# Performance work log

Hardware: AMD Instinct MI355X
Metric: run time of the kernel (lower is better)

## Reference

```python
import jax, jax.numpy as jnp
import numpy as np

EPS = 1e-6
SIGMA = 1.0       # get_matrix default sigma
INIT_SIGMA = 1.0  # args.init_sigma


def setup_inputs() -> dict:
    key = jax.random.key(0)
    ks = jax.random.split(key, 12)
    B, T, LD, NB = 16, 2048, 256, 32
    s = 1.0 / np.sqrt(LD)
    E_raw = jax.random.normal(ks[5], (LD, LD), jnp.float32)
    E_w, _ = jnp.linalg.qr(E_raw)  # orthogonal like geotorch.orthogonal
    return {
        "Z": jax.random.normal(ks[0], (B, T, LD), jnp.float32),
        "obs_times": jax.random.uniform(ks[1], (B, T, 1), jnp.float32),
        "D": jax.random.normal(ks[2], (NB, LD), jnp.float32),
        "coeff_W": jax.random.normal(ks[3], (NB, LD), jnp.float32) * s,
        "coeff_b": jnp.zeros((NB,), jnp.float32),
        "E_w": E_w.astype(jnp.float32),
        "B_w": jax.random.normal(ks[6], (LD, LD), jnp.float32) * s,
        "C_w": jax.random.normal(ks[7], (LD, LD), jnp.float32) * s,
        "M_w": jax.random.normal(ks[8], (LD, LD), jnp.float32) * s,
        "init_mean_p": jax.random.normal(ks[9], (LD,), jnp.float32),
        "init_log_var": jax.random.normal(ks[10], (LD,), jnp.float32),
        "y_log_var": jax.random.normal(ks[11], (LD,), jnp.float32),
    }


def _binop(qi, qj):
    # (A_j*A_i, Bu_j + A_j*Bu_i): combine earlier element qi with later qj
    A_i, Bu_i = qi
    A_j, Bu_j = qj
    return (A_j * A_i, Bu_j + A_j * Bu_i)


def reference(Z, obs_times, D, coeff_W, coeff_b, E_w, B_w, C_w, M_w,
              init_mean_p, init_log_var, y_log_var):
    LD = Z.shape[-1]
    # alphas = B(Z)
    alphas = jnp.einsum('btd,ed->bte', Z, B_w)                      # (B,T,LD)
    # get_matrix (vectorized over batch and time)
    A_basis = -(jnp.exp(D) + EPS)                                   # (NB,LD), negative
    A_coeff = jax.nn.softmax(jnp.einsum('btd,nd->btn', alphas, coeff_W) + coeff_b, axis=-1)
    A_mat = jnp.einsum('btn,nd->btd', A_coeff, A_basis)             # (B,T,LD)
    exp_A_m = jnp.exp(A_mat * obs_times)                            # mean transition
    exp_B_m = (exp_A_m - 1.0) / A_mat * alphas
    exp_A_v = jnp.exp(2.0 * A_mat * obs_times)                      # var transition
    exp_B_v = 0.5 * SIGMA ** 2 * (exp_A_v - 1.0) / A_mat + EPS
    mats_A = jnp.concatenate([exp_A_m, exp_A_v], axis=-1)           # (B,T,2LD)
    mats_B = jnp.concatenate([exp_B_m, exp_B_v], axis=-1)           # (B,T,2LD)
    # parallel linear-recurrence scan over time
    cum_A, cum_B = jax.lax.associative_scan(_binop, (mats_A, mats_B), axis=1)
    # initial condition in rotated coordinates
    init_mean0 = E_w.T @ init_mean_p                                # (LD,)
    diag_v = INIT_SIGMA * (jnp.exp(init_log_var) + EPS)
    init_var0 = jnp.einsum('ki,k->i', E_w ** 2, diag_v)             # diag(E^T diag(v) E)
    init_mv = jnp.concatenate([init_mean0, init_var0], axis=0)      # (2LD,)
    imv = cum_A * init_mv                                           # (B,T,2LD)
    init_mean, init_var = imv[..., :LD], imv[..., LD:]
    xs_mean, xs_var = cum_B[..., :LD], cum_B[..., LD:]
    y_var = jnp.exp(y_log_var) + EPS
    # output projections: M(E(.)) and history C(E(Z))
    history = jnp.einsum('btd,ed,fe->btf', Z, E_w, C_w)
    means = jnp.einsum('btd,ed,fe->btf', xs_mean + init_mean, E_w, M_w) + history
    stds = jnp.einsum('btd,ed,fe->btf', jnp.sqrt(xs_var + init_var + y_var), E_w, M_w)
    return means, stds, alphas
```

## Files before the change

kernel.cpp:

```cpp
#include <hip/hip_runtime.h>
#include <math.h>

#define EPS 1e-6f

#define B_   16
#define T_   2048
#define LD   256
#define NB   32
#define BT   (B_ * T_)
#define NCH  64
#define CHUNK (T_ / NCH)

typedef short bf16x8 __attribute__((ext_vector_type(8)));
typedef float f32x4  __attribute__((ext_vector_type(4)));

__device__ __forceinline__ unsigned short f2b(float f) {
    unsigned int u = __float_as_uint(f);
    unsigned int r = (u + 0x7fffu + ((u >> 16) & 1u)) >> 16;
    return (unsigned short)r;
}

__device__ __forceinline__ float b2f(unsigned short h) {
    return __uint_as_float(((unsigned int)h) << 16);
}

__device__ __forceinline__ void gl_lds16(const void* g, void* l) {
    __builtin_amdgcn_global_load_lds(
        (const __attribute__((address_space(1))) unsigned int*)g,
        (__attribute__((address_space(3))) unsigned int*)l, 16, 0, 0);
}

__device__ __forceinline__ int xcd_map(int wg) {
    int x = wg & 7, s = wg >> 3;
    return (s & 3) | (x << 2) | ((s >> 2) << 5);
}

__device__ __forceinline__ void stage_tile(const unsigned short* __restrict__ src,
                                           int row0, int stride, int kb,
                                           unsigned short* lds, int wv, int lane) {
#pragma unroll
    for (int cc = 0; cc < 2; ++cc) {
        int c = wv * 2 + cc;
        int r = c * 16 + (lane >> 2);
        int qd = (lane & 3) ^ ((r >> 1) & 3);
        const unsigned short* g = src + (size_t)(row0 + r) * stride + kb + qd * 8;
        gl_lds16(g, lds + c * 512);
    }
}

__device__ __forceinline__ bf16x8 frag_ld(const unsigned short* lds, int row, int qd) {
    int pq = qd ^ ((row >> 1) & 3);
    return *(const bf16x8*)(lds + row * 32 + pq * 8);
}

__device__ __forceinline__ int u_idx(int i, int d) {
    return ((d >> 5) << 10) + (i << 5) + (((((d >> 3) & 3)) ^ (i & 3)) << 3) + (d & 7);
}

__global__ __launch_bounds__(256) void k_pre(const float* __restrict__ Z,
                                             const float* __restrict__ Dm,
                                             const float* __restrict__ cw,
                                             const float* __restrict__ Ew,
                                             const float* __restrict__ Bw,
                                             const float* __restrict__ Cw,
                                             const float* __restrict__ Mw,
                                             const float* __restrict__ imp,
                                             const float* __restrict__ ilv,
                                             const float* __restrict__ ylv,
                                             unsigned short* __restrict__ GMh,
                                             unsigned short* __restrict__ GCh,
                                             unsigned short* __restrict__ cwbh,
                                             float* __restrict__ im0,
                                             float* __restrict__ iv0,
                                             float* __restrict__ yv,
                                             unsigned short* __restrict__ AbTh,
                                             unsigned short* __restrict__ AbTl,
                                             unsigned short* __restrict__ Bwh,
                                             unsigned short* __restrict__ Zh) {
    int bid = blockIdx.x;
    int tid = threadIdx.x;
    if (bid < 544) {
        const float* W; const float* E; unsigned short* out; int d0, f0;
        if (bid < 256)      { W = Mw; E = Ew; out = GMh;  d0 = (bid & 15) * 16; f0 = (bid >> 4) * 16; }
        else if (bid < 512) { W = Cw; E = Ew; out = GCh;  d0 = (bid & 15) * 16; f0 = ((bid - 256) >> 4) * 16; }
        else                { W = cw; E = Bw; out = cwbh; d0 = (bid & 15) * 16; f0 = ((bid - 512) >> 4) * 16; }
        __shared__ float Ws[16][17];
        __shared__ float Es[16][17];
        int tx = tid & 15, ty = tid >> 4;
        float acc = 0.f;
        for (int eb = 0; eb < LD; eb += 16) {
            Ws[ty][tx] = W[(f0 + ty) * LD + eb + tx];
            Es[ty][tx] = E[(eb + ty) * LD + d0 + tx];
            __syncthreads();
#pragma unroll
            for (int k = 0; k < 16; ++k) acc = fmaf(Ws[ty][k], Es[k][tx], acc);
            __syncthreads();
        }
        out[(f0 + ty) * LD + d0 + tx] = f2b(acc);
    } else if (bid < 577) {
        int sub = bid - 544;
        int t = tid;
        if (sub == 0) {
            float sm = 0.f, sv = 0.f;
            for (int k = 0; k < LD; ++k) {
                float e = Ew[k * LD + t];
                sm = fmaf(e, imp[k], sm);
                sv = fmaf(e * e, expf(ilv[k]) + EPS, sv);
            }
            im0[t] = sm;
            iv0[t] = sv;
            yv[t]  = expf(ylv[t]) + EPS;
        } else {
            int n = sub - 1;
            float a = -(expf(Dm[n * LD + t]) + EPS);
            unsigned short h = f2b(a);
            AbTh[t * NB + n] = h;
            AbTl[t * NB + n] = f2b(a - b2f(h));
        }
    } else if (bid < 641) {
        int i = (bid - 577) * 256 + tid;
        float4 v = ((const float4*)Bw)[i];
        ((ushort4*)Bwh)[i] = make_ushort4(f2b(v.x), f2b(v.y), f2b(v.z), f2b(v.w));
    } else {
        int i = (bid - 641) * 256 + tid;
        float4 v = ((const float4*)Z)[i];
        ((ushort4*)Zh)[i] = make_ushort4(f2b(v.x), f2b(v.y), f2b(v.z), f2b(v.w));
    }
}

__global__ __launch_bounds__(256) void k_zb(const unsigned short* __restrict__ Zh,
                                            const unsigned short* __restrict__ Bwh,
                                            const unsigned short* __restrict__ cwbh,
                                            const float* __restrict__ cb,
                                            float* __restrict__ alphas,
                                            float* __restrict__ logits) {
    __shared__ unsigned short As[128 * 32];
    __shared__ unsigned short Bs[128 * 32];
    int tid = threadIdx.x, lane = tid & 63, wv = tid >> 6;
    int m0 = blockIdx.x * 128;
    int y  = blockIdx.y;
    if (y < 2) {
        int n0 = y * 128;
        int wm = (wv & 1) * 64, wn = (wv >> 1) * 64;
        f32x4 acc[4][4];
#pragma unroll
        for (int i = 0; i < 4; ++i)
#pragma unroll
            for (int j = 0; j < 4; ++j) acc[i][j] = (f32x4){0.f, 0.f, 0.f, 0.f};
        for (int kb = 0; kb < LD; kb += 32) {
            stage_tile(Zh, m0, LD, kb, As, wv, lane);
            stage_tile(Bwh, n0, LD, kb, Bs, wv, lane);
            __syncthreads();
            int qd = lane >> 4;
            bf16x8 af[4], bf[4];
#pragma unroll
            for (int i = 0; i < 4; ++i) af[i] = frag_ld(As, wm + i * 16 + (lane & 15), qd);
#pragma unroll
            for (int j = 0; j < 4; ++j) bf[j] = frag_ld(Bs, wn + j * 16 + (lane & 15), qd);
#pragma unroll
            for (int i = 0; i < 4; ++i)
#pragma unroll
                for (int j = 0; j < 4; ++j)
                    acc[i][j] = __builtin_amdgcn_mfma_f32_16x16x32_bf16(af[i], bf[j], acc[i][j], 0, 0, 0);
            __syncthreads();
        }
        int col = wn + (lane & 15);
        int rb  = wm + ((lane >> 4) << 2);
#pragma unroll
        for (int i = 0; i < 4; ++i)
#pragma unroll
            for (int j = 0; j < 4; ++j)
#pragma unroll
                for (int r = 0; r < 4; ++r)
                    alphas[(size_t)(m0 + rb + i * 16 + r) * LD + n0 + col + j * 16] = acc[i][j][r];
    } else {
        f32x4 acc[2][2];
#pragma unroll
        for (int i = 0; i < 2; ++i)
#pragma unroll
            for (int j = 0; j < 2; ++j) acc[i][j] = (f32x4){0.f, 0.f, 0.f, 0.f};
        for (int kb = 0; kb < LD; kb += 32) {
            stage_tile(Zh, m0, LD, kb, As, wv, lane);
            if (wv < 2) {
                int r = wv * 16 + (lane >> 2);
                int qd = (lane & 3) ^ ((r >> 1) & 3);
                gl_lds16(cwbh + (size_t)r * LD + kb + qd * 8, Bs + wv * 512);
            }
            __syncthreads();
            int qd = lane >> 4;
            bf16x8 af[2], bff[2];
#pragma unroll
            for (int i = 0; i < 2; ++i) af[i] = frag_ld(As, wv * 32 + i * 16 + (lane & 15), qd);
#pragma unroll
            for (int j = 0; j < 2; ++j) bff[j] = frag_ld(Bs, j * 16 + (lane & 15), qd);
#pragma unroll
            for (int i = 0; i < 2; ++i)
#pragma unroll
                for (int j = 0; j < 2; ++j)
                    acc[i][j] = __builtin_amdgcn_mfma_f32_16x16x32_bf16(af[i], bff[j], acc[i][j], 0, 0, 0);
            __syncthreads();
        }
        int col = lane & 15;
        int rb  = (lane >> 4) << 2;
#pragma unroll
        for (int i = 0; i < 2; ++i)
#pragma unroll
            for (int j = 0; j < 2; ++j)
#pragma unroll
                for (int r = 0; r < 4; ++r) {
                    int row = m0 + wv * 32 + i * 16 + rb + r;
                    int cc  = j * 16 + col;
                    logits[(size_t)row * NB + cc] = acc[i][j][r] + cb[cc];
                }
    }
}

__global__ __launch_bounds__(256) void k_tot(const float* __restrict__ logits,
                                             const float* __restrict__ alphas,
                                             const float* __restrict__ obs,
                                             const unsigned short* __restrict__ AbTh,
                                             const unsigned short* __restrict__ AbTl,
                                             float* __restrict__ totA,
                                             float* __restrict__ totBm,
                                             float* __restrict__ totBv) {
    __shared__ unsigned int U[8192];
    __shared__ unsigned short Ph[1024];
    __shared__ unsigned short Pl[1024];
    int tid = threadIdx.x;
    int d = tid;
    int bid = xcd_map(blockIdx.x);
    int bt0 = bid * CHUNK;

    float av[32];
#pragma unroll
    for (int i = 0; i < 32; ++i) av[i] = alphas[(size_t)(bt0 + i) * LD + d];

    int l = tid & 31, rg = tid >> 5;
#pragma unroll
    for (int jj = 0; jj < 4; ++jj) {
        int row = rg * 4 + jj;
        float v = logits[(size_t)(bt0 + row) * NB + l];
        float mx = v;
#pragma unroll
        for (int off = 16; off >= 1; off >>= 1) mx = fmaxf(mx, __shfl_xor(mx, off, 32));
        float e = __expf(v - mx);
        float s = e;
#pragma unroll
        for (int off = 16; off >= 1; off >>= 1) s += __shfl_xor(s, off, 32);
        float p = e * __builtin_amdgcn_rcpf(s);
        unsigned short h = f2b(p);
        unsigned short lo = f2b(p - b2f(h));
        int sa = row * 32 + ((((l >> 3) ^ ((row >> 1) & 3))) << 3) + (l & 7);
        Ph[sa] = h;
        Pl[sa] = lo;
    }
    __syncthreads();

    int lane = tid & 63, wv = tid >> 6;
    int qd = lane >> 4, mr = lane & 15;
    bf16x8 ph[2], pl[2];
#pragma unroll
    for (int iT = 0; iT < 2; ++iT) {
        ph[iT] = frag_ld(Ph, iT * 16 + mr, qd);
        pl[iT] = frag_ld(Pl, iT * 16 + mr, qd);
    }
#pragma unroll
    for (int j = 0; j < 4; ++j) {
        int dcol = wv * 64 + j * 16 + mr;
        bf16x8 ah = *(const bf16x8*)(AbTh + dcol * NB + qd * 8);
        bf16x8 al = *(const bf16x8*)(AbTl + dcol * NB + qd * 8);
#pragma unroll
        for (int iT = 0; iT < 2; ++iT) {
            f32x4 acc = (f32x4){0.f, 0.f, 0.f, 0.f};
            acc = __builtin_amdgcn_mfma_f32_16x16x32_bf16(ph[iT], ah, acc, 0, 0, 0);
            acc = __builtin_amdgcn_mfma_f32_16x16x32_bf16(pl[iT], ah, acc, 0, 0, 0);
            acc = __builtin_amdgcn_mfma_f32_16x16x32_bf16(ph[iT], al, acc, 0, 0, 0);
#pragma unroll
            for (int r = 0; r < 4; ++r)
                U[u_idx(iT * 16 + qd * 4 + r, dcol)] = __float_as_uint(acc[r]);
        }
    }
    __syncthreads();

    float ra = 1.f, rm = 0.f, rv = 0.f;
    int ubase = ((d >> 5) << 10) + (d & 7);
    int qb = (d >> 3) & 3;
#pragma unroll
    for (int i = 0; i < CHUNK; ++i) {
        int ui = ubase + (i << 5) + ((qb ^ (i & 3)) << 3);
        float Am = __uint_as_float(U[ui]);
        float tt = obs[bt0 + i];
        float eAm = __expf(Am * tt);
        float ieA = __builtin_amdgcn_rcpf(Am);
        float e2  = eAm * eAm;
        float eBm = (eAm - 1.f) * ieA * av[i];
        float eBv = fmaf(0.5f * (e2 - 1.f), ieA, EPS);
        rm = fmaf(eAm, rm, eBm);
        rv = fmaf(e2, rv, eBv);
        ra *= eAm;
    }
    int pidx = bid * LD + d;
    totA[pidx] = ra; totBm[pidx] = rm; totBv[pidx] = rv;
}

__global__ __launch_bounds__(256) void k_chunkpfx(const float* __restrict__ totA,
                                                  const float* __restrict__ totBm,
                                                  const float* __restrict__ totBv,
                                                  float* __restrict__ preA,
                                                  float* __restrict__ preBm,
                                                  float* __restrict__ preBv) {
    int d = threadIdx.x;
    int b = blockIdx.x;
    float Pa = 1.f, Pm = 0.f, Pv = 0.f;
    for (int g = 0; g < 8; ++g) {
        float a8[8], m8[8], v8[8];
#pragma unroll
        for (int k = 0; k < 8; ++k) {
            int pidx = (b * NCH + g * 8 + k) * LD + d;
            a8[k] = totA[pidx]; m8[k] = totBm[pidx]; v8[k] = totBv[pidx];
        }
#pragma unroll
        for (int k = 0; k < 8; ++k) {
            int pidx = (b * NCH + g * 8 + k) * LD + d;
            preA[pidx] = Pa; preBm[pidx] = Pm; preBv[pidx] = Pv;
            Pm = fmaf(a8[k], Pm, m8[k]);
            Pv = fmaf(a8[k] * a8[k], Pv, v8[k]);
            Pa *= a8[k];
        }
    }
}

__global__ __launch_bounds__(256) void k_sms(const float* __restrict__ logits,
                                             const float* __restrict__ alphas,
                                             const float* __restrict__ obs,
                                             const unsigned short* __restrict__ AbTh,
                                             const unsigned short* __restrict__ AbTl,
                                             const float* __restrict__ preA,
                                             const float* __restrict__ preBm,
                                             const float* __restrict__ preBv,
                                             const float* __restrict__ im0,
                                             const float* __restrict__ iv0,
                                             const float* __restrict__ yv,
                                             const unsigned short* __restrict__ Zh,
                                             const unsigned short* __restrict__ GMh,
                                             const unsigned short* __restrict__ GCh,
                                             float* __restrict__ means,
                                             float* __restrict__ stds) {
    __shared__ unsigned int U[16384];
    unsigned short* Ph = (unsigned short*)U;
    unsigned short* Pl = (unsigned short*)(U + 1024);
    int tid = threadIdx.x, lane = tid & 63, wv = tid >> 6;
    int d = tid;
    int bt0 = blockIdx.x * 64;

    int l = tid & 31, rg = tid >> 5;
#pragma unroll
    for (int jj = 0; jj < 8; ++jj) {
        int row = rg * 8 + jj;
        float v = logits[(size_t)(bt0 + row) * NB + l];
        float mx = v;
#pragma unroll
        for (int off = 16; off >= 1; off >>= 1) mx = fmaxf(mx, __shfl_xor(mx, off, 32));
        float e = __expf(v - mx);
        float s = e;
#pragma unroll
        for (int off = 16; off >= 1; off >>= 1) s += __shfl_xor(s, off, 32);
        float p = e * __builtin_amdgcn_rcpf(s);
        unsigned short h = f2b(p);
        unsigned short lo = f2b(p - b2f(h));
        int sa = row * 32 + ((((l >> 3) ^ ((row >> 1) & 3))) << 3) + (l & 7);
        Ph[sa] = h;
        Pl[sa] = lo;
    }
    __syncthreads();

    int qd = lane >> 4, mr = lane & 15;
    bf16x8 ph[4], pl[4];
#pragma unroll
    for (int iT = 0; iT < 4; ++iT) {
        ph[iT] = frag_ld(Ph, iT * 16 + mr, qd);
        pl[iT] = frag_ld(Pl, iT * 16 + mr, qd);
    }
    __syncthreads();

#pragma unroll
    for (int j = 0; j < 4; ++j) {
        int dcol = wv * 64 + j * 16 + mr;
        bf16x8 ah = *(const bf16x8*)(AbTh + dcol * NB + qd * 8);
        bf16x8 al = *(const bf16x8*)(AbTl + dcol * NB + qd * 8);
#pragma unroll
        for (int iT = 0; iT < 4; ++iT) {
            f32x4 acc = (f32x4){0.f, 0.f, 0.f, 0.f};
            acc = __builtin_amdgcn_mfma_f32_16x16x32_bf16(ph[iT], ah, acc, 0, 0, 0);
            acc = __builtin_amdgcn_mfma_f32_16x16x32_bf16(pl[iT], ah, acc, 0, 0, 0);
            acc = __builtin_amdgcn_mfma_f32_16x16x32_bf16(ph[iT], al, acc, 0, 0, 0);
#pragma unroll
            for (int r = 0; r < 4; ++r) {
                int i = iT * 16 + qd * 4 + r;
                U[((i >> 5) << 13) + u_idx(i & 31, dcol)] = __float_as_uint(acc[r]);
            }
        }
    }
    __syncthreads();

    int p0 = (blockIdx.x * 2) * LD + d;
    float ga0 = preA[p0],      gm0 = preBm[p0],      gv0 = preBv[p0];
    float ga1 = preA[p0 + LD], gm1 = preBm[p0 + LD], gv1 = preBv[p0 + LD];
    float i0 = im0[d], v0 = iv0[d], yvd = yv[d];

    int ubase = ((d >> 5) << 10) + (d & 7);
    int qb = (d >> 3) & 3;
    for (int g = 0; g < 4; ++g) {
        float av0[8], av1[8];
#pragma unroll
        for (int k = 0; k < 8; ++k) {
            av0[k] = alphas[(size_t)(bt0 + g * 8 + k) * LD + d];
            av1[k] = alphas[(size_t)(bt0 + 32 + g * 8 + k) * LD + d];
        }
#pragma unroll
        for (int k = 0; k < 8; ++k) {
            int i = g * 8 + k;
            int ui0 = ubase + (i << 5) + ((qb ^ (i & 3)) << 3);
            int ui1 = 8192 + ui0;
            float Am0 = __uint_as_float(U[ui0]);
            float Am1 = __uint_as_float(U[ui1]);
            float t0 = obs[bt0 + i];
            float t1 = obs[bt0 + 32 + i];
            float e0 = __expf(Am0 * t0);
            float e1 = __expf(Am1 * t1);
            float r0 = __builtin_amdgcn_rcpf(Am0);
            float r1 = __builtin_amdgcn_rcpf(Am1);
            float q0 = e0 * e0, q1 = e1 * e1;
            float bm0 = (e0 - 1.f) * r0 * av0[k];
            float bm1 = (e1 - 1.f) * r1 * av1[k];
            float bv0 = fmaf(0.5f * (q0 - 1.f), r0, EPS);
            float bv1 = fmaf(0.5f * (q1 - 1.f), r1, EPS);
            gm0 = fmaf(e0, gm0, bm0);   gm1 = fmaf(e1, gm1, bm1);
            gv0 = fmaf(q0, gv0, bv0);   gv1 = fmaf(q1, gv1, bv1);
            ga0 *= e0;                  ga1 *= e1;
            float mm0 = fmaf(ga0, i0, gm0);
            float mm1 = fmaf(ga1, i0, gm1);
            float vv0 = fmaf(ga0 * ga0, v0, gv0) + yvd;
            float vv1 = fmaf(ga1 * ga1, v0, gv1) + yvd;
            float ss0 = sqrtf(vv0);
            float ss1 = sqrtf(vv1);
            U[ui0] = ((unsigned int)f2b(mm0) << 16) | (unsigned int)f2b(ss0);
            U[ui1] = ((unsigned int)f2b(mm1) << 16) | (unsigned int)f2b(ss1);
        }
    }
    __syncthreads();

    f32x4 accm[4][4], accs[4][4];
#pragma unroll
    for (int iT = 0; iT < 4; ++iT)
#pragma unroll
        for (int j = 0; j < 4; ++j) {
            accm[iT][j] = (f32x4){0.f, 0.f, 0.f, 0.f};
            accs[iT][j] = (f32x4){0.f, 0.f, 0.f, 0.f};
        }
    for (int kc = 0; kc < 8; ++kc) {
        bf16x8 am[4], asv[4], az[4];
#pragma unroll
        for (int iT = 0; iT < 4; ++iT) {
            int row = iT * 16 + mr;
            int ii = row & 31;
            int off = ((row >> 5) << 13) + (kc << 10) + (ii << 5) + ((qd ^ (ii & 3)) << 3);
            uint4 ua = *(const uint4*)(U + off);
            uint4 ub = *(const uint4*)(U + off + 4);
            unsigned int uu[8] = {ua.x, ua.y, ua.z, ua.w, ub.x, ub.y, ub.z, ub.w};
            bf16x8 m_, s_;
#pragma unroll
            for (int k = 0; k < 8; ++k) {
                m_[k] = (short)(uu[k] >> 16);
                s_[k] = (short)(uu[k] & 0xffffu);
            }
            am[iT] = m_; asv[iT] = s_;
            az[iT] = *(const bf16x8*)(Zh + (size_t)(bt0 + row) * LD + kc * 32 + qd * 8);
        }
#pragma unroll
        for (int j = 0; j < 4; ++j) {
            int brow = wv * 64 + j * 16 + mr;
            bf16x8 bm = *(const bf16x8*)(GMh + (size_t)brow * LD + kc * 32 + qd * 8);
            bf16x8 bc = *(const bf16x8*)(GCh + (size_t)brow * LD + kc * 32 + qd * 8);
#pragma unroll
            for (int iT = 0; iT < 4; ++iT) {
                accm[iT][j] = __builtin_amdgcn_mfma_f32_16x16x32_bf16(am[iT],  bm, accm[iT][j], 0, 0, 0);
                accs[iT][j] = __builtin_amdgcn_mfma_f32_16x16x32_bf16(asv[iT], bm, accs[iT][j], 0, 0, 0);
                accm[iT][j] = __builtin_amdgcn_mfma_f32_16x16x32_bf16(az[iT],  bc, accm[iT][j], 0, 0, 0);
            }
        }
    }

    int col0 = wv * 64 + mr;
    int rb   = (lane >> 4) << 2;
#pragma unroll
    for (int iT = 0; iT < 4; ++iT)
#pragma unroll
        for (int j = 0; j < 4; ++j)
#pragma unroll
            for (int r = 0; r < 4; ++r) {
                size_t off = (size_t)(bt0 + iT * 16 + rb + r) * LD + col0 + j * 16;
                means[off] = accm[iT][j][r];
                stds[off]  = accs[iT][j][r];
            }
}

extern "C" void kernel_launch(void* const* d_in, const int* in_sizes, int n_in,
                              void* d_out, int out_size, void* d_ws, size_t ws_size,
                              hipStream_t stream) {
    const float* Z   = (const float*)d_in[0];
    const float* obs = (const float*)d_in[1];
    const float* Dm  = (const float*)d_in[2];
    const float* cw  = (const float*)d_in[3];
    const float* cb  = (const float*)d_in[4];
    const float* Ew  = (const float*)d_in[5];
    const float* Bw  = (const float*)d_in[6];
    const float* Cw  = (const float*)d_in[7];
    const float* Mw  = (const float*)d_in[8];
    const float* imp = (const float*)d_in[9];
    const float* ilv = (const float*)d_in[10];
    const float* ylv = (const float*)d_in[11];

    float* out    = (float*)d_out;
    float* means  = out;
    float* stds   = out + (size_t)BT * LD;
    float* alphas = out + (size_t)2 * BT * LD;

    char* ws = (char*)d_ws;
    size_t o = 0;
    unsigned short* Zh   = (unsigned short*)(ws + o); o += (size_t)BT * LD * 2;
    float*          logits=(float*)(ws + o);          o += (size_t)BT * NB * 4;
    unsigned short* GMh  = (unsigned short*)(ws + o); o += (size_t)LD * LD * 2;
    unsigned short* GCh  = (unsigned short*)(ws + o); o += (size_t)LD * LD * 2;
    unsigned short* Bwh  = (unsigned short*)(ws + o); o += (size_t)LD * LD * 2;
    unsigned short* cwbh = (unsigned short*)(ws + o); o += (size_t)NB * LD * 2;
    unsigned short* AbTh = (unsigned short*)(ws + o); o += (size_t)LD * NB * 2;
    unsigned short* AbTl = (unsigned short*)(ws + o); o += (size_t)LD * NB * 2;
    float* totA  = (float*)(ws + o); o += (size_t)B_ * NCH * LD * 4;
    float* totBm = (float*)(ws + o); o += (size_t)B_ * NCH * LD * 4;
    float* totBv = (float*)(ws + o); o += (size_t)B_ * NCH * LD * 4;
    float* preA  = (float*)(ws + o); o += (size_t)B_ * NCH * LD * 4;
    float* preBm = (float*)(ws + o); o += (size_t)B_ * NCH * LD * 4;
    float* preBv = (float*)(ws + o); o += (size_t)B_ * NCH * LD * 4;
    float* im0   = (float*)(ws + o); o += LD * 4;
    float* iv0   = (float*)(ws + o); o += LD * 4;
    float* yv    = (float*)(ws + o); o += LD * 4;

    k_pre<<<dim3(641 + BT * LD / 1024), dim3(256), 0, stream>>>(
        Z, Dm, cw, Ew, Bw, Cw, Mw, imp, ilv, ylv,
        GMh, GCh, cwbh, im0, iv0, yv, AbTh, AbTl, Bwh, Zh);

    k_zb<<<dim3(BT / 128, 3), dim3(256), 0, stream>>>(Zh, Bwh, cwbh, cb, alphas, logits);

    k_tot<<<dim3(B_ * NCH), dim3(256), 0, stream>>>(logits, alphas, obs, AbTh, AbTl,
                                                    totA, totBm, totBv);
    k_chunkpfx<<<dim3(B_), dim3(LD), 0, stream>>>(totA, totBm, totBv, preA, preBm, preBv);

    k_sms<<<dim3(B_ * NCH / 2), dim3(256), 0, stream>>>(logits, alphas, obs, AbTh, AbTl,
                                                        preA, preBm, preBv,
                                                        im0, iv0, yv,
                                                        Zh, GMh, GCh, means, stds);
}
```

Baseline: 234.5 us.

## Cache A_mat from chunk-total pass and drop LDS staging in Z·B GEMM

```diff
diff --git a/kernel.cpp b/kernel.cpp
--- a/kernel.cpp
+++ b/kernel.cpp
@@ -24,28 +24,9 @@
     return __uint_as_float(((unsigned int)h) << 16);
 }
 
-__device__ __forceinline__ void gl_lds16(const void* g, void* l) {
-    __builtin_amdgcn_global_load_lds(
-        (const __attribute__((address_space(1))) unsigned int*)g,
-        (__attribute__((address_space(3))) unsigned int*)l, 16, 0, 0);
-}
-
 __device__ __forceinline__ int xcd_map(int wg) {
     int x = wg & 7, s = wg >> 3;
     return (s & 3) | (x << 2) | ((s >> 2) << 5);
-}
-
-__device__ __forceinline__ void stage_tile(const unsigned short* __restrict__ src,
-                                           int row0, int stride, int kb,
-                                           unsigned short* lds, int wv, int lane) {
-#pragma unroll
-    for (int cc = 0; cc < 2; ++cc) {
-        int c = wv * 2 + cc;
-        int r = c * 16 + (lane >> 2);
-        int qd = (lane & 3) ^ ((r >> 1) & 3);
-        const unsigned short* g = src + (size_t)(row0 + r) * stride + kb + qd * 8;
-        gl_lds16(g, lds + c * 512);
-    }
 }
 
 __device__ __forceinline__ bf16x8 frag_ld(const unsigned short* lds, int row, int qd) {
@@ -134,9 +115,8 @@
                                             const float* __restrict__ cb,
                                             float* __restrict__ alphas,
                                             float* __restrict__ logits) {
-    __shared__ unsigned short As[128 * 32];
-    __shared__ unsigned short Bs[128 * 32];
     int tid = threadIdx.x, lane = tid & 63, wv = tid >> 6;
+    int qd = lane >> 4, mr = lane & 15;
     int m0 = blockIdx.x * 128;
     int y  = blockIdx.y;
     if (y < 2) {
@@ -148,24 +128,21 @@
 #pragma unroll
             for (int j = 0; j < 4; ++j) acc[i][j] = (f32x4){0.f, 0.f, 0.f, 0.f};
         for (int kb = 0; kb < LD; kb += 32) {
-            stage_tile(Zh, m0, LD, kb, As, wv, lane);
-            stage_tile(Bwh, n0, LD, kb, Bs, wv, lane);
-            __syncthreads();
-            int qd = lane >> 4;
             bf16x8 af[4], bf[4];
 #pragma unroll
-            for (int i = 0; i < 4; ++i) af[i] = frag_ld(As, wm + i * 16 + (lane & 15), qd);
-#pragma unroll
-            for (int j = 0; j < 4; ++j) bf[j] = frag_ld(Bs, wn + j * 16 + (lane & 15), qd);
+            for (int i = 0; i < 4; ++i)
+                af[i] = *(const bf16x8*)(Zh + (size_t)(m0 + wm + i * 16 + mr) * LD + kb + qd * 8);
+#pragma unroll
+            for (int j = 0; j < 4; ++j)
+                bf[j] = *(const bf16x8*)(Bwh + (size_t)(n0 + wn + j * 16 + mr) * LD + kb + qd * 8);
 #pragma unroll
             for (int i = 0; i < 4; ++i)
 #pragma unroll
                 for (int j = 0; j < 4; ++j)
                     acc[i][j] = __builtin_amdgcn_mfma_f32_16x16x32_bf16(af[i], bf[j], acc[i][j], 0, 0, 0);
-            __syncthreads();
-        }
-        int col = wn + (lane & 15);
-        int rb  = wm + ((lane >> 4) << 2);
+        }
+        int col = wn + mr;
+        int rb  = wm + (qd << 2);
 #pragma unroll
         for (int i = 0; i < 4; ++i)
 #pragma unroll
@@ -180,28 +157,21 @@
 #pragma unroll
             for (int j = 0; j < 2; ++j) acc[i][j] = (f32x4){0.f, 0.f, 0.f, 0.f};
         for (int kb = 0; kb < LD; kb += 32) {
-            stage_tile(Zh, m0, LD, kb, As, wv, lane);
-            if (wv < 2) {
-                int r = wv * 16 + (lane >> 2);
-                int qd = (lane & 3) ^ ((r >> 1) & 3);
-                gl_lds16(cwbh + (size_t)r * LD + kb + qd * 8, Bs + wv * 512);
-            }
-            __syncthreads();
-            int qd = lane >> 4;
             bf16x8 af[2], bff[2];
 #pragma unroll
-            for (int i = 0; i < 2; ++i) af[i] = frag_ld(As, wv * 32 + i * 16 + (lane & 15), qd);
-#pragma unroll
-            for (int j = 0; j < 2; ++j) bff[j] = frag_ld(Bs, j * 16 + (lane & 15), qd);
+            for (int i = 0; i < 2; ++i)
+                af[i] = *(const bf16x8*)(Zh + (size_t)(m0 + wv * 32 + i * 16 + mr) * LD + kb + qd * 8);
+#pragma unroll
+            for (int j = 0; j < 2; ++j)
+                bff[j] = *(const bf16x8*)(cwbh + (size_t)(j * 16 + mr) * LD + kb + qd * 8);
 #pragma unroll
             for (int i = 0; i < 2; ++i)
 #pragma unroll
                 for (int j = 0; j < 2; ++j)
                     acc[i][j] = __builtin_amdgcn_mfma_f32_16x16x32_bf16(af[i], bff[j], acc[i][j], 0, 0, 0);
-            __syncthreads();
-        }
-        int col = lane & 15;
-        int rb  = (lane >> 4) << 2;
+        }
+        int col = mr;
+        int rb  = qd << 2;
 #pragma unroll
         for (int i = 0; i < 2; ++i)
 #pragma unroll
@@ -220,6 +190,7 @@
                                              const float* __restrict__ obs,
                                              const unsigned short* __restrict__ AbTh,
                                              const unsigned short* __restrict__ AbTl,
+                                             float* __restrict__ AmT,
                                              float* __restrict__ totA,
                                              float* __restrict__ totBm,
                                              float* __restrict__ totBv) {
@@ -278,6 +249,7 @@
 #pragma unroll
             for (int r = 0; r < 4; ++r)
                 U[u_idx(iT * 16 + qd * 4 + r, dcol)] = __float_as_uint(acc[r]);
+            *(f32x4*)(AmT + (size_t)bid * (LD * 32) + (size_t)dcol * 32 + iT * 16 + qd * 4) = acc;
         }
     }
     __syncthreads();
@@ -325,16 +297,14 @@
             preA[pidx] = Pa; preBm[pidx] = Pm; preBv[pidx] = Pv;
             Pm = fmaf(a8[k], Pm, m8[k]);
             Pv = fmaf(a8[k] * a8[k], Pv, v8[k]);
-            Pa *= a8[k];
-        }
-    }
-}
-
-__global__ __launch_bounds__(256) void k_sms(const float* __restrict__ logits,
-                                             const float* __restrict__ alphas,
+            Pa = a8[k] * Pa;
+        }
+    }
+}
+
+__global__ __launch_bounds__(256) void k_sms(const float* __restrict__ alphas,
                                              const float* __restrict__ obs,
-                                             const unsigned short* __restrict__ AbTh,
-                                             const unsigned short* __restrict__ AbTl,
+                                             const float* __restrict__ AmT,
                                              const float* __restrict__ preA,
                                              const float* __restrict__ preBm,
                                              const float* __restrict__ preBv,
@@ -347,66 +317,19 @@
                                              float* __restrict__ means,
                                              float* __restrict__ stds) {
     __shared__ unsigned int U[16384];
-    unsigned short* Ph = (unsigned short*)U;
-    unsigned short* Pl = (unsigned short*)(U + 1024);
     int tid = threadIdx.x, lane = tid & 63, wv = tid >> 6;
     int d = tid;
     int bt0 = blockIdx.x * 64;
-
-    int l = tid & 31, rg = tid >> 5;
-#pragma unroll
-    for (int jj = 0; jj < 8; ++jj) {
-        int row = rg * 8 + jj;
-        float v = logits[(size_t)(bt0 + row) * NB + l];
-        float mx = v;
-#pragma unroll
-        for (int off = 16; off >= 1; off >>= 1) mx = fmaxf(mx, __shfl_xor(mx, off, 32));
-        float e = __expf(v - mx);
-        float s = e;
-#pragma unroll
-        for (int off = 16; off >= 1; off >>= 1) s += __shfl_xor(s, off, 32);
-        float p = e * __builtin_amdgcn_rcpf(s);
-        unsigned short h = f2b(p);
-        unsigned short lo = f2b(p - b2f(h));
-        int sa = row * 32 + ((((l >> 3) ^ ((row >> 1) & 3))) << 3) + (l & 7);
-        Ph[sa] = h;
-        Pl[sa] = lo;
-    }
-    __syncthreads();
-
+    int c0  = blockIdx.x * 2;
     int qd = lane >> 4, mr = lane & 15;
-    bf16x8 ph[4], pl[4];
-#pragma unroll
-    for (int iT = 0; iT < 4; ++iT) {
-        ph[iT] = frag_ld(Ph, iT * 16 + mr, qd);
-        pl[iT] = frag_ld(Pl, iT * 16 + mr, qd);
-    }
-    __syncthreads();
-
-#pragma unroll
-    for (int j = 0; j < 4; ++j) {
-        int dcol = wv * 64 + j * 16 + mr;
-        bf16x8 ah = *(const bf16x8*)(AbTh + dcol * NB + qd * 8);
-        bf16x8 al = *(const bf16x8*)(AbTl + dcol * NB + qd * 8);
-#pragma unroll
-        for (int iT = 0; iT < 4; ++iT) {
-            f32x4 acc = (f32x4){0.f, 0.f, 0.f, 0.f};
-            acc = __builtin_amdgcn_mfma_f32_16x16x32_bf16(ph[iT], ah, acc, 0, 0, 0);
-            acc = __builtin_amdgcn_mfma_f32_16x16x32_bf16(pl[iT], ah, acc, 0, 0, 0);
-            acc = __builtin_amdgcn_mfma_f32_16x16x32_bf16(ph[iT], al, acc, 0, 0, 0);
-#pragma unroll
-            for (int r = 0; r < 4; ++r) {
-                int i = iT * 16 + qd * 4 + r;
-                U[((i >> 5) << 13) + u_idx(i & 31, dcol)] = __float_as_uint(acc[r]);
-            }
-        }
-    }
-    __syncthreads();
-
-    int p0 = (blockIdx.x * 2) * LD + d;
+
+    int p0 = c0 * LD + d;
     float ga0 = preA[p0],      gm0 = preBm[p0],      gv0 = preBv[p0];
     float ga1 = preA[p0 + LD], gm1 = preBm[p0 + LD], gv1 = preBv[p0 + LD];
     float i0 = im0[d], v0 = iv0[d], yvd = yv[d];
+
+    const float* A0 = AmT + (size_t)c0 * (LD * 32) + (size_t)d * 32;
+    const float* A1 = A0 + (size_t)(LD * 32);
 
     int ubase = ((d >> 5) << 10) + (d & 7);
     int qb = (d >> 3) & 3;
@@ -417,13 +340,19 @@
             av0[k] = alphas[(size_t)(bt0 + g * 8 + k) * LD + d];
             av1[k] = alphas[(size_t)(bt0 + 32 + g * 8 + k) * LD + d];
         }
+        f32x4 a0a = *(const f32x4*)(A0 + g * 8);
+        f32x4 a0b = *(const f32x4*)(A0 + g * 8 + 4);
+        f32x4 a1a = *(const f32x4*)(A1 + g * 8);
+        f32x4 a1b = *(const f32x4*)(A1 + g * 8 + 4);
+        float am0[8] = {a0a[0], a0a[1], a0a[2], a0a[3], a0b[0], a0b[1], a0b[2], a0b[3]};
+        float am1[8] = {a1a[0], a1a[1], a1a[2], a1a[3], a1b[0], a1b[1], a1b[2], a1b[3]};
 #pragma unroll
         for (int k = 0; k < 8; ++k) {
             int i = g * 8 + k;
             int ui0 = ubase + (i << 5) + ((qb ^ (i & 3)) << 3);
             int ui1 = 8192 + ui0;
-            float Am0 = __uint_as_float(U[ui0]);
-            float Am1 = __uint_as_float(U[ui1]);
+            float Am0 = am0[k];
+            float Am1 = am1[k];
             float t0 = obs[bt0 + i];
             float t1 = obs[bt0 + 32 + i];
             float e0 = __expf(Am0 * t0);
@@ -530,6 +459,7 @@
     size_t o = 0;
     unsigned short* Zh   = (unsigned short*)(ws + o); o += (size_t)BT * LD * 2;
     float*          logits=(float*)(ws + o);          o += (size_t)BT * NB * 4;
+    float*          AmT  = (float*)(ws + o);          o += (size_t)BT * LD * 4;
     unsigned short* GMh  = (unsigned short*)(ws + o); o += (size_t)LD * LD * 2;
     unsigned short* GCh  = (unsigned short*)(ws + o); o += (size_t)LD * LD * 2;
     unsigned short* Bwh  = (unsigned short*)(ws + o); o += (size_t)LD * LD * 2;
@@ -553,10 +483,10 @@
     k_zb<<<dim3(BT / 128, 3), dim3(256), 0, stream>>>(Zh, Bwh, cwbh, cb, alphas, logits);
 
     k_tot<<<dim3(B_ * NCH), dim3(256), 0, stream>>>(logits, alphas, obs, AbTh, AbTl,
-                                                    totA, totBm, totBv);
+                                                    AmT, totA, totBm, totBv);
     k_chunkpfx<<<dim3(B_), dim3(LD), 0, stream>>>(totA, totBm, totBv, preA, preBm, preBv);
 
-    k_sms<<<dim3(B_ * NCH / 2), dim3(256), 0, stream>>>(logits, alphas, obs, AbTh, AbTl,
+    k_sms<<<dim3(B_ * NCH / 2), dim3(256), 0, stream>>>(alphas, obs, AmT,
                                                         preA, preBm, preBv,
                                                         im0, iv0, yv,
                                                         Zh, GMh, GCh, means, stds);
```

Measured after the change: 251.3 us. 7.2% more time.
